# Kernel optimization log

Measured on AMD Instinct MI355X. Metric: run time of the kernel, lower is better.

Reference implementation:

```python
import jax, jax.numpy as jnp
import numpy as np
import math

B, T, D = 2, 2048, 1024
H, HD = 16, 64          # num_heads, head_dim = D // H
ROPE, BASE = 64, 10000.0  # rope covers full head dim
GLOBAL_IDS = jnp.array([2, 3, 4, 5, 6, 7], dtype=jnp.int32)


def setup_inputs() -> dict:
    key = jax.random.key(0)
    k1, k2, k3, k4 = jax.random.split(key, 4)
    x = jax.random.normal(k1, (B, T, D), dtype=jnp.float32)
    input_ids = jax.random.randint(k2, (B, T), 0, 1024, dtype=jnp.int32)
    W_qkv = jax.random.normal(k3, (3 * H * HD, D), dtype=jnp.float32) * 0.02
    b_qkv = jnp.zeros((3 * H * HD,), dtype=jnp.float32)
    W_out = jax.random.normal(k4, (D, H * HD), dtype=jnp.float32) * 0.02
    b_out = jnp.zeros((D,), dtype=jnp.float32)
    return {"x": x, "input_ids": input_ids, "W_qkv": W_qkv, "b_qkv": b_qkv,
            "W_out": W_out, "b_out": b_out}


def _apply_rotary(x, cos, sin):
    # x: [B,H,T,HD]; rope covers first ROPE dims (= full head here)
    x_rot, x_pass = x[..., :ROPE], x[..., ROPE:]
    half = ROPE // 2
    x1, x2 = x_rot[..., :half], x_rot[..., half:]
    x1n = x1 * cos - x2 * sin
    x2n = x1 * sin + x2 * cos
    return jnp.concatenate([x1n, x2n, x_pass], axis=-1)


def reference(x, input_ids, W_qkv, b_qkv, W_out, b_out):
    Bx, Tx, _ = x.shape
    qkv = x @ W_qkv.T + b_qkv                      # [B,T,3*H*HD]
    q, k, v = jnp.split(qkv, 3, axis=-1)
    def heads(t):
        return t.reshape(Bx, Tx, H, HD).transpose(0, 2, 1, 3)  # [B,H,T,HD]
    q, k, v = heads(q), heads(k), heads(v)

    # RoPE
    pos = jnp.arange(Tx, dtype=jnp.float32)
    inv_freq = 1.0 / (BASE ** (jnp.arange(0, ROPE, 2, dtype=jnp.float32) / ROPE))
    freqs = pos[:, None] * inv_freq[None, :]        # [T, ROPE//2]
    cos, sin = jnp.cos(freqs)[None, None], jnp.sin(freqs)[None, None]
    q = _apply_rotary(q, cos, sin)
    k = _apply_rotary(k, cos, sin)

    # causal mask OR global-query rows (BigBird-style)
    causal = jnp.tril(jnp.ones((Tx, Tx), dtype=bool))[None, None]   # [1,1,T,T]
    global_mask = jnp.isin(input_ids, GLOBAL_IDS)                    # [B,T]
    allow = causal | global_mask[:, None, :, None]                   # [B,1,T,T]

    scale = math.sqrt(HD)
    logits = jnp.einsum('bhqd,bhkd->bhqk', q, k) / scale
    neg = -jnp.finfo(logits.dtype).max
    logits = jnp.where(allow, logits, neg)
    attn = jax.nn.softmax(logits, axis=-1)
    out = jnp.einsum('bhqk,bhkd->bhqd', attn, v)
    out = out.transpose(0, 2, 1, 3).reshape(Bx, Tx, H * HD)
    return out @ W_out.T + b_out
```

## Files before the change

### kernel.cpp

```cpp
#include <hip/hip_runtime.h>
#include <math.h>

#define Bc 2
#define Tc 2048
#define Dc 1024
#define Hc 16
#define HDc 64

typedef __attribute__((ext_vector_type(8))) short bf16x8;
typedef __attribute__((ext_vector_type(4))) float f32x4;
typedef __attribute__((ext_vector_type(16))) float f32x16;

__device__ __forceinline__ unsigned short f2bf(float f) {
    union { float f; unsigned int u; } v; v.f = f;
    unsigned int r = (v.u + 0x7FFFu + ((v.u >> 16) & 1u)) >> 16;
    return (unsigned short)r;
}
__device__ __forceinline__ unsigned pack2bf(float a, float b) {
    unsigned au = __float_as_uint(a) + 0x8000u;
    unsigned bu = __float_as_uint(b) + 0x8000u;
    return __builtin_amdgcn_perm(bu, au, 0x07060302u);
}

#define CEXP 0.1803368801111204f

__global__ __launch_bounds__(256) void convert_bf16(
    const float* __restrict__ x, const float* __restrict__ wqkv,
    const float* __restrict__ wout,
    unsigned short* __restrict__ xb, unsigned short* __restrict__ wqkvb,
    unsigned short* __restrict__ woutb, float2* __restrict__ ropeTab)
{
    const int gid = blockIdx.x * 256 + threadIdx.x;
    if (gid < Tc * 32) {
        const int t = gid >> 5, i = gid & 31;
        const float freq = exp2f((float)i * -0.4152410118609203f);
        const float ang = (float)t * freq;
        ropeTab[gid] = make_float2(cosf(ang), sinf(ang));
    }
    const int i = gid * 4;
    const float* src; unsigned short* dst; int off;
    if (i < 4194304)      { src = x;    dst = xb;    off = i; }
    else if (i < 7340032) { src = wqkv; dst = wqkvb; off = i - 4194304; }
    else                  { src = wout; dst = woutb; off = i - 7340032; }
    float4 v = *(const float4*)&src[off];
    ushort4 o;
    o.x = f2bf(v.x); o.y = f2bf(v.y); o.z = f2bf(v.z); o.w = f2bf(v.w);
    *(ushort4*)&dst[off] = o;
}

template <int MODE>
__global__ __launch_bounds__(256) void gemm_mfma(
    const unsigned short* __restrict__ A, const unsigned short* __restrict__ W,
    const float* __restrict__ bias, float* __restrict__ C,
    unsigned short* __restrict__ Qp, unsigned short* __restrict__ Kp,
    unsigned short* __restrict__ Vtp, const float2* __restrict__ ropeTab,
    int M, int N, int K)
{
    __shared__ unsigned short Apk[128 * 8 * 8];
    __shared__ unsigned short Bpk[128 * 8 * 8];

    const int tid = threadIdx.x;
    const int lane = tid & 63;
    const int wave = tid >> 6;
    const int quad = lane >> 4;
    const int c = lane & 15;
    const int wm = wave >> 1;
    const int wn = wave & 1;
    const int m0 = blockIdx.y * 128;
    const int n0 = blockIdx.x * 128;

    f32x4 acc[4][4];
#pragma unroll
    for (int mt = 0; mt < 4; mt++)
#pragma unroll
        for (int nt = 0; nt < 4; nt++) acc[mt][nt] = (f32x4){0.f, 0.f, 0.f, 0.f};

    const int soct = tid & 7;
    const int srow0 = tid >> 3;

    for (int k0 = 0; k0 < K; k0 += 64) {
        __syncthreads();
#pragma unroll
        for (int it = 0; it < 4; it++) {
            const int row = srow0 + it * 32;
            bf16x8 av = *(const bf16x8*)&A[(size_t)(m0 + row) * K + k0 + soct * 8];
            *(bf16x8*)&Apk[(row * 8 + (soct ^ (row & 7))) * 8] = av;
            bf16x8 wv = *(const bf16x8*)&W[(size_t)(n0 + row) * K + k0 + soct * 8];
            *(bf16x8*)&Bpk[(row * 8 + (soct ^ (row & 7))) * 8] = wv;
        }
        __syncthreads();
#pragma unroll
        for (int ko = 0; ko < 2; ko++) {
            bf16x8 af[4], bf[4];
#pragma unroll
            for (int mt = 0; mt < 4; mt++) {
                const int m = wm * 64 + mt * 16 + c;
                af[mt] = *(const bf16x8*)&Apk[(m * 8 + ((ko * 4 + quad) ^ (m & 7))) * 8];
            }
#pragma unroll
            for (int nt = 0; nt < 4; nt++) {
                const int n = wn * 64 + nt * 16 + c;
                bf[nt] = *(const bf16x8*)&Bpk[(n * 8 + ((ko * 4 + quad) ^ (n & 7))) * 8];
            }
#pragma unroll
            for (int mt = 0; mt < 4; mt++)
#pragma unroll
                for (int nt = 0; nt < 4; nt++)
                    acc[mt][nt] = __builtin_amdgcn_mfma_f32_16x16x32_bf16(
                        af[mt], bf[nt], acc[mt][nt], 0, 0, 0);
        }
    }

    if (MODE == 0) {
#pragma unroll
        for (int mt = 0; mt < 4; mt++) {
            const int m = m0 + wm * 64 + mt * 16 + quad * 4;
#pragma unroll
            for (int nt = 0; nt < 4; nt++) {
                const int n = n0 + wn * 64 + nt * 16 + c;
                const float bv = bias[n];
#pragma unroll
                for (int reg = 0; reg < 4; reg++)
                    C[(size_t)(m + reg) * N + n] = acc[mt][nt][reg] + bv;
            }
        }
    } else {
        const int n_wave = n0 + wn * 64;
        const int which = n_wave >> 10;
        const int h = (n_wave >> 6) & 15;
        const int b = m0 >> 11;
        const int t_base = (m0 & 2047) + wm * 64;

        __syncthreads();
        unsigned short* stg = ((wave < 2) ? Apk : Bpk) + (wave & 1) * 4096;

        if (which < 2) {
            unsigned short* dst = (which == 0) ? Qp : Kp;
#pragma unroll
            for (int mt = 0; mt < 4; mt++) {
#pragma unroll
                for (int nt = 0; nt < 2; nt++) {
                    const int i1 = nt * 16 + c;
                    const float bv1 = bias[n_wave + i1];
                    const float bv2 = bias[n_wave + 32 + i1];
#pragma unroll
                    for (int reg = 0; reg < 4; reg++) {
                        const int row = mt * 16 + quad * 4 + reg;
                        const float2 cs = ropeTab[(t_base + row) * 32 + i1];
                        const float x1 = acc[mt][nt][reg] + bv1;
                        const float x2 = acc[mt][nt + 2][reg] + bv2;
                        const int col2 = 32 + i1;
                        stg[(row * 8 + ((i1 >> 3) ^ (row & 7))) * 8 + (i1 & 7)] =
                            f2bf(x1 * cs.x - x2 * cs.y);
                        stg[(row * 8 + ((col2 >> 3) ^ (row & 7))) * 8 + (col2 & 7)] =
                            f2bf(x1 * cs.y + x2 * cs.x);
                    }
                }
            }
            const size_t obase = ((size_t)(b * Hc + h) * Tc + t_base) * HDc;
            const int oct = lane & 7;
#pragma unroll
            for (int k = 0; k < 8; k++) {
                const int f = lane * 8 + k * 512;
                const int row = f >> 6;
                bf16x8 vv = *(const bf16x8*)&stg[(row * 8 + (oct ^ (row & 7))) * 8];
                *(bf16x8*)&dst[obase + f] = vv;
            }
        } else {
#pragma unroll
            for (int mt = 0; mt < 4; mt++) {
#pragma unroll
                for (int nt = 0; nt < 4; nt++) {
                    const int d = nt * 16 + c;
                    const float bv = bias[n_wave + d];
#pragma unroll
                    for (int reg = 0; reg < 4; reg++) {
                        const int r = mt * 16 + quad * 4 + reg;
                        stg[(d * 8 + ((r >> 3) ^ (d & 7))) * 8 + (r & 7)] =
                            f2bf(acc[mt][nt][reg] + bv);
                    }
                }
            }
            const size_t vbase = (size_t)(b * Hc + h) * HDc * Tc;
            const int oct = lane & 7;
#pragma unroll
            for (int k = 0; k < 8; k++) {
                const int d = (lane >> 3) + k * 8;
                bf16x8 vv = *(const bf16x8*)&stg[(d * 8 + (oct ^ (d & 7))) * 8];
                *(bf16x8*)&Vtp[vbase + (size_t)d * Tc + t_base + oct * 8] = vv;
            }
        }
    }
}

__global__ __launch_bounds__(256) void attn_fused(
    const unsigned short* __restrict__ Q, const unsigned short* __restrict__ K,
    const unsigned short* __restrict__ Vt, const int* __restrict__ ids,
    unsigned short* __restrict__ AO)
{
    __shared__ float smem[8448];

    const int tid = threadIdx.x;
    const int lane = tid & 63;
    const int wave = tid >> 6;
    const int c32 = lane & 31;
    const int h = lane >> 5;
    const int blk = blockIdx.x;

    if (blk < 32) {
        int* s_list = (int*)smem;
        int* s_cnt = (int*)smem + 64;
        float* s_accm = smem + 128;
        float* s_lm = s_accm + 8192;

        const int bh = blk;
        const int b = bh >> 4;
        const int hd = bh & 15;
        const size_t qkbase = (size_t)bh * Tc * HDc;

        if (tid == 0) *s_cnt = 0;
        __syncthreads();
        for (int i = tid; i < Tc; i += 256) {
            int id = ids[b * Tc + i];
            if ((unsigned)(id - 2) <= 5u) {
                int p = atomicAdd(s_cnt, 1);
                if (p < 64) s_list[p] = i;
            }
        }
        __syncthreads();
        const int cnt = min(*s_cnt, 64);

        for (int pass = 0; pass * 32 < cnt; pass++) {
            const int slot = pass * 32 + c32;
            const int row = (slot < cnt) ? s_list[slot] : s_list[0];

            bf16x8 qf[4];
#pragma unroll
            for (int ko = 0; ko < 4; ko++)
                qf[ko] = *(const bf16x8*)&Q[qkbase + (size_t)row * HDc + ko * 16 + h * 8];

            f32x16 acc0 = {}, acc1 = {};
            float lacc = 0.0f;

            for (int it = wave; it < Tc / 64; it += 4) {
                const int t0 = it * 64;
                f32x16 s0 = {}, s1 = {};
#pragma unroll
                for (int ko = 0; ko < 4; ko++) {
                    const int koff = ko * 16 + h * 8;
                    bf16x8 kf0 = *(const bf16x8*)&K[qkbase + (size_t)(t0 + c32) * HDc + koff];
                    bf16x8 kf1 = *(const bf16x8*)&K[qkbase + (size_t)(t0 + 32 + c32) * HDc + koff];
                    s0 = __builtin_amdgcn_mfma_f32_32x32x16_bf16(kf0, qf[ko], s0, 0, 0, 0);
                    s1 = __builtin_amdgcn_mfma_f32_32x32x16_bf16(kf1, qf[ko], s1, 0, 0, 0);
                }
                float v[32];
#pragma unroll
                for (int r = 0; r < 16; r++) { v[r] = s0[r]; v[16 + r] = s1[r]; }
#pragma unroll
                for (int i = 0; i < 32; i++) v[i] = exp2f(v[i] * CEXP);
                unsigned pk[16];
#pragma unroll
                for (int i = 0; i < 16; i++) pk[i] = pack2bf(v[2 * i], v[2 * i + 1]);
#pragma unroll
                for (int st = 1; st < 32; st <<= 1)
#pragma unroll
                    for (int i = 0; i < 32; i += 2 * st) v[i] += v[i + st];
                lacc += v[0];
#pragma unroll
                for (int ko = 0; ko < 4; ko++) {
                    const int a = (ko >> 1) * 8 + (ko & 1) * 4;
                    unsigned keep0 = h ? pk[a + 2] : pk[a + 0];
                    unsigned keep1 = h ? pk[a + 3] : pk[a + 1];
                    unsigned send0 = h ? pk[a + 0] : pk[a + 2];
                    unsigned send1 = h ? pk[a + 1] : pk[a + 3];
                    unsigned recv0 = (unsigned)__shfl_xor((int)send0, 32);
                    unsigned recv1 = (unsigned)__shfl_xor((int)send1, 32);
                    union { bf16x8 v8; unsigned u[4]; } pf;
                    pf.u[0] = h ? recv0 : keep0;
                    pf.u[1] = h ? recv1 : keep1;
                    pf.u[2] = h ? keep0 : recv0;
                    pf.u[3] = h ? keep1 : recv1;
                    const int oct = ko * 2 + h;
                    bf16x8 vf0 = *(const bf16x8*)&Vt[qkbase + (size_t)c32 * Tc + t0 + oct * 8];
                    bf16x8 vf1 = *(const bf16x8*)&Vt[qkbase + (size_t)(32 + c32) * Tc + t0 + oct * 8];
                    acc0 = __builtin_amdgcn_mfma_f32_32x32x16_bf16(vf0, pf.v8, acc0, 0, 0, 0);
                    acc1 = __builtin_amdgcn_mfma_f32_32x32x16_bf16(vf1, pf.v8, acc1, 0, 0, 0);
                }
            }

            const float lfull = lacc + __shfl_xor(lacc, 32);
            if (h == 0) s_lm[wave * 32 + c32] = lfull;
#pragma unroll
            for (int r = 0; r < 16; r++) {
                const int d = (r & 3) + 8 * (r >> 2) + 4 * h;
                s_accm[(wave * 64 + d) * 32 + c32] = acc0[r];
                s_accm[(wave * 64 + 32 + d) * 32 + c32] = acc1[r];
            }
            __syncthreads();
            for (int i = tid; i < 2048; i += 256) {
                const int sl = i >> 6, d = i & 63;
                if (pass * 32 + sl < cnt) {
                    const float o = s_accm[(0 * 64 + d) * 32 + sl] + s_accm[(1 * 64 + d) * 32 + sl] +
                                    s_accm[(2 * 64 + d) * 32 + sl] + s_accm[(3 * 64 + d) * 32 + sl];
                    const float lt = s_lm[sl] + s_lm[32 + sl] + s_lm[64 + sl] + s_lm[96 + sl];
                    const int qrow = s_list[pass * 32 + sl];
                    AO[((size_t)(b * Tc + qrow)) * Dc + hd * HDc + d] = f2bf(o / lt);
                }
            }
            __syncthreads();
        }
        return;
    }

    unsigned short* KV = (unsigned short*)smem;

    const int idx = blk - 32;
    const int bh = idx & 31;
    const int b = bh >> 4;
    const int hd = bh & 15;
    const int qi = 31 - (idx >> 5);
    const int qb0 = qi * 64;
    const int qsub = wave & 1;
    const int par = wave >> 1;
    const int wq0 = qb0 + qsub * 32;
    const size_t qkbase = (size_t)bh * Tc * HDc;
    const int q = wq0 + c32;

    bf16x8 qf[4];
#pragma unroll
    for (int ko = 0; ko < 4; ko++)
        qf[ko] = *(const bf16x8*)&Q[qkbase + (size_t)q * HDc + ko * 16 + h * 8];

    const int myid = ids[b * Tc + q];
    const bool gr = ((unsigned)(myid - 2) <= 5u);

    f32x16 acc0 = {}, acc1 = {};
    float lacc = 0.0f;

    const int nIter = qi + 1;
    const int skey = tid >> 3;
    const int soct = tid & 7;

    bf16x8 kA0, kA1, vA0, vA1, kB0, kB1, vB0, vB1;

    auto loadT = [&](int t0, bf16x8& k0, bf16x8& k1, bf16x8& v0, bf16x8& v1) {
        const int r0 = skey, r1 = skey + 32;
        k0 = *(const bf16x8*)&K[qkbase + (size_t)(t0 + r0) * HDc + soct * 8];
        k1 = *(const bf16x8*)&K[qkbase + (size_t)(t0 + r1) * HDc + soct * 8];
        v0 = *(const bf16x8*)&Vt[qkbase + (size_t)r0 * Tc + t0 + soct * 8];
        v1 = *(const bf16x8*)&Vt[qkbase + (size_t)r1 * Tc + t0 + soct * 8];
    };
    auto writeT = [&](int buf, bf16x8 k0, bf16x8 k1, bf16x8 v0, bf16x8 v1) {
        const int r0 = skey, r1 = skey + 32;
        unsigned short* Kb = KV + buf * 4096;
        unsigned short* Vb = KV + 8192 + buf * 4096;
        *(bf16x8*)&Kb[(r0 * 8 + (soct ^ (r0 & 7))) * 8] = k0;
        *(bf16x8*)&Kb[(r1 * 8 + (soct ^ (r1 & 7))) * 8] = k1;
        *(bf16x8*)&Vb[(r0 * 8 + (soct ^ (r0 & 7))) * 8] = v0;
        *(bf16x8*)&Vb[(r1 * 8 + (soct ^ (r1 & 7))) * 8] = v1;
    };

    auto compute = [&](int buf, int t0) {
        if (((t0 >> 6) & 1) != par) return;
        const unsigned short* Kb = KV + buf * 4096;
        const unsigned short* Vb = KV + 8192 + buf * 4096;

        f32x16 s0 = {}, s1 = {};
#pragma unroll
        for (int ko = 0; ko < 4; ko++) {
            const int oct = ko * 2 + h;
            const int k0i = c32;
            const int k1i = 32 + c32;
            bf16x8 kf0 = *(const bf16x8*)&Kb[(k0i * 8 + (oct ^ (k0i & 7))) * 8];
            bf16x8 kf1 = *(const bf16x8*)&Kb[(k1i * 8 + (oct ^ (k1i & 7))) * 8];
            s0 = __builtin_amdgcn_mfma_f32_32x32x16_bf16(kf0, qf[ko], s0, 0, 0, 0);
            s1 = __builtin_amdgcn_mfma_f32_32x32x16_bf16(kf1, qf[ko], s1, 0, 0, 0);
        }

        float v[32];
#pragma unroll
        for (int r = 0; r < 16; r++) { v[r] = s0[r]; v[16 + r] = s1[r]; }
#pragma unroll
        for (int i = 0; i < 32; i++) v[i] = exp2f(v[i] * CEXP);

        const bool needMask = (t0 + 63 > wq0);
        if (needMask) {
            const int thr = wq0 + c32 - t0 - 4 * h;
#pragma unroll
            for (int kt = 0; kt < 2; kt++)
#pragma unroll
                for (int r = 0; r < 16; r++) {
                    const int ckr = kt * 32 + (r & 3) + 8 * (r >> 2);
                    v[kt * 16 + r] = (ckr <= thr) ? v[kt * 16 + r] : 0.0f;
                }
        }

        unsigned pk[16];
#pragma unroll
        for (int i = 0; i < 16; i++) pk[i] = pack2bf(v[2 * i], v[2 * i + 1]);

#pragma unroll
        for (int st = 1; st < 32; st <<= 1)
#pragma unroll
            for (int i = 0; i < 32; i += 2 * st) v[i] += v[i + st];
        lacc += v[0];

#pragma unroll
        for (int ko = 0; ko < 4; ko++) {
            const int a = (ko >> 1) * 8 + (ko & 1) * 4;
            unsigned keep0 = h ? pk[a + 2] : pk[a + 0];
            unsigned keep1 = h ? pk[a + 3] : pk[a + 1];
            unsigned send0 = h ? pk[a + 0] : pk[a + 2];
            unsigned send1 = h ? pk[a + 1] : pk[a + 3];
            unsigned recv0 = (unsigned)__shfl_xor((int)send0, 32);
            unsigned recv1 = (unsigned)__shfl_xor((int)send1, 32);
            union { bf16x8 v8; unsigned u[4]; } pf;
            pf.u[0] = h ? recv0 : keep0;
            pf.u[1] = h ? recv1 : keep1;
            pf.u[2] = h ? keep0 : recv0;
            pf.u[3] = h ? keep1 : recv1;
            const int oct = ko * 2 + h;
            const int d0 = c32, d1 = 32 + c32;
            bf16x8 vf0 = *(const bf16x8*)&Vb[(d0 * 8 + (oct ^ (d0 & 7))) * 8];
            bf16x8 vf1 = *(const bf16x8*)&Vb[(d1 * 8 + (oct ^ (d1 & 7))) * 8];
            acc0 = __builtin_amdgcn_mfma_f32_32x32x16_bf16(vf0, pf.v8, acc0, 0, 0, 0);
            acc1 = __builtin_amdgcn_mfma_f32_32x32x16_bf16(vf1, pf.v8, acc1, 0, 0, 0);
        }
    };

    loadT(0, kA0, kA1, vA0, vA1);
    writeT(0, kA0, kA1, vA0, vA1);
    for (int it = 0; ; it += 2) {
        __syncthreads();
        const bool p1 = (it + 1) < nIter;
        if (p1) loadT((it + 1) * 64, kB0, kB1, vB0, vB1);
        compute(0, it * 64);
        if (!p1) break;
        writeT(1, kB0, kB1, vB0, vB1);
        __syncthreads();
        const bool p2 = (it + 2) < nIter;
        if (p2) loadT((it + 2) * 64, kA0, kA1, vA0, vA1);
        compute(1, (it + 1) * 64);
        if (!p2) break;
        writeT(0, kA0, kA1, vA0, vA1);
    }

    const float lw_ = lacc + __shfl_xor(lacc, 32);
    __syncthreads();
    float* mrg = smem;
    float* lmr = smem + 4096;
    if (wave >= 2) {
        const int s = wave - 2;
#pragma unroll
        for (int r = 0; r < 16; r++) {
            const int d = (r & 3) + 8 * (r >> 2) + 4 * h;
            mrg[(s * 64 + d) * 32 + c32] = acc0[r];
            mrg[(s * 64 + 32 + d) * 32 + c32] = acc1[r];
        }
        if (h == 0) lmr[s * 32 + c32] = lw_;
    }
    __syncthreads();
    if (wave < 2 && !gr) {
        const float l = lw_ + lmr[wave * 32 + c32];
        const float inv = 1.0f / l;
        unsigned short* dst = &AO[((size_t)(b * Tc + q)) * Dc + hd * HDc];
#pragma unroll
        for (int i = 0; i < 8; i++) {
            const int r = 2 * i;
            const int d = (r & 3) + 8 * (r >> 2) + 4 * h;
            const float a0 = acc0[r]     + mrg[(wave * 64 + d) * 32 + c32];
            const float a1 = acc0[r + 1] + mrg[(wave * 64 + d + 1) * 32 + c32];
            const float b0 = acc1[r]     + mrg[(wave * 64 + 32 + d) * 32 + c32];
            const float b1 = acc1[r + 1] + mrg[(wave * 64 + 32 + d + 1) * 32 + c32];
            *(unsigned*)&dst[d]      = pack2bf(a0 * inv, a1 * inv);
            *(unsigned*)&dst[32 + d] = pack2bf(b0 * inv, b1 * inv);
        }
    }
}

extern "C" void kernel_launch(void* const* d_in, const int* in_sizes, int n_in,
                              void* d_out, int out_size, void* d_ws, size_t ws_size,
                              hipStream_t stream)
{
    const float* x    = (const float*)d_in[0];
    const int*   ids  = (const int*)d_in[1];
    const float* Wqkv = (const float*)d_in[2];
    const float* bqkv = (const float*)d_in[3];
    const float* Wout = (const float*)d_in[4];
    const float* bout = (const float*)d_in[5];
    float* out = (float*)d_out;

    const size_t TEN = (size_t)Bc * Hc * Tc * HDc;
    unsigned short* xb    = (unsigned short*)d_ws;
    unsigned short* wqkvb = xb + 4194304;
    unsigned short* woutb = wqkvb + 3145728;
    float2* ropeTab       = (float2*)(woutb + 1048576);
    unsigned short* Qb    = (unsigned short*)(ropeTab + 65536);
    unsigned short* Kb    = Qb + TEN;
    unsigned short* Vtb   = Kb + TEN;
    unsigned short* AOb   = Vtb + TEN;

    convert_bf16<<<8192, 256, 0, stream>>>(x, Wqkv, Wout, xb, wqkvb, woutb,
                                           ropeTab);
    dim3 g1(3072 / 128, 4096 / 128);
    gemm_mfma<1><<<g1, 256, 0, stream>>>(xb, wqkvb, bqkv, nullptr,
                                         Qb, Kb, Vtb, ropeTab, 4096, 3072, 1024);
    attn_fused<<<1056, 256, 0, stream>>>(Qb, Kb, Vtb, ids, AOb);
    dim3 g4(1024 / 128, 4096 / 128);
    gemm_mfma<0><<<g4, 256, 0, stream>>>(AOb, woutb, bout, out,
                                         nullptr, nullptr, nullptr, nullptr,
                                         4096, 1024, 1024);
}
```

Before: 220.4 us.

## Give each wave its own 32-query block and stream K/V directly from global

The causal attention path drops the shared-memory K/V staging, the block-level double buffer and the cross-wave partial-sum merge. Each wave now owns one 32-row query group and walks every key tile itself, loading K fragments from global one tile ahead and V fragments straight into registers. The grid shrinks from 1056 to 544 blocks. This removes the __syncthreads barriers and the LDS merge, but each wave now reads the full K/V stream on its own, which multiplies global/L2 traffic and exposes more load latency. Register pressure also rises.

```diff
diff --git a/kernel.cpp b/kernel.cpp
--- a/kernel.cpp
+++ b/kernel.cpp
@@ -312,17 +312,12 @@
         return;
     }
 
-    unsigned short* KV = (unsigned short*)smem;
-
-    const int idx = blk - 32;
-    const int bh = idx & 31;
+    const int widx = (blk - 32) * 4 + wave;
+    const int bh = widx & 31;
     const int b = bh >> 4;
     const int hd = bh & 15;
-    const int qi = 31 - (idx >> 5);
-    const int qb0 = qi * 64;
-    const int qsub = wave & 1;
-    const int par = wave >> 1;
-    const int wq0 = qb0 + qsub * 32;
+    const int qg = 63 - (widx >> 5);
+    const int wq0 = qg * 32;
     const size_t qkbase = (size_t)bh * Tc * HDc;
     const int q = wq0 + c32;
 
@@ -336,45 +331,38 @@
 
     f32x16 acc0 = {}, acc1 = {};
     float lacc = 0.0f;
-
-    const int nIter = qi + 1;
-    const int skey = tid >> 3;
-    const int soct = tid & 7;
-
-    bf16x8 kA0, kA1, vA0, vA1, kB0, kB1, vB0, vB1;
-
-    auto loadT = [&](int t0, bf16x8& k0, bf16x8& k1, bf16x8& v0, bf16x8& v1) {
-        const int r0 = skey, r1 = skey + 32;
-        k0 = *(const bf16x8*)&K[qkbase + (size_t)(t0 + r0) * HDc + soct * 8];
-        k1 = *(const bf16x8*)&K[qkbase + (size_t)(t0 + r1) * HDc + soct * 8];
-        v0 = *(const bf16x8*)&Vt[qkbase + (size_t)r0 * Tc + t0 + soct * 8];
-        v1 = *(const bf16x8*)&Vt[qkbase + (size_t)r1 * Tc + t0 + soct * 8];
-    };
-    auto writeT = [&](int buf, bf16x8 k0, bf16x8 k1, bf16x8 v0, bf16x8 v1) {
-        const int r0 = skey, r1 = skey + 32;
-        unsigned short* Kb = KV + buf * 4096;
-        unsigned short* Vb = KV + 8192 + buf * 4096;
-        *(bf16x8*)&Kb[(r0 * 8 + (soct ^ (r0 & 7))) * 8] = k0;
-        *(bf16x8*)&Kb[(r1 * 8 + (soct ^ (r1 & 7))) * 8] = k1;
-        *(bf16x8*)&Vb[(r0 * 8 + (soct ^ (r0 & 7))) * 8] = v0;
-        *(bf16x8*)&Vb[(r1 * 8 + (soct ^ (r1 & 7))) * 8] = v1;
-    };
-
-    auto compute = [&](int buf, int t0) {
-        if (((t0 >> 6) & 1) != par) return;
-        const unsigned short* Kb = KV + buf * 4096;
-        const unsigned short* Vb = KV + 8192 + buf * 4096;
-
-        f32x16 s0 = {}, s1 = {};
+    const int nIter = (qg >> 1) + 1;
+
+    bf16x8 kcur[8], knext[8], vcur[8];
+#pragma unroll
+    for (int ko = 0; ko < 4; ko++) {
+        const int koff = ko * 16 + h * 8;
+        kcur[ko * 2 + 0] = *(const bf16x8*)&K[qkbase + (size_t)c32 * HDc + koff];
+        kcur[ko * 2 + 1] = *(const bf16x8*)&K[qkbase + (size_t)(32 + c32) * HDc + koff];
+    }
+
+    for (int it = 0; it < nIter; it++) {
+        const int t0 = it * 64;
 #pragma unroll
         for (int ko = 0; ko < 4; ko++) {
             const int oct = ko * 2 + h;
-            const int k0i = c32;
-            const int k1i = 32 + c32;
-            bf16x8 kf0 = *(const bf16x8*)&Kb[(k0i * 8 + (oct ^ (k0i & 7))) * 8];
-            bf16x8 kf1 = *(const bf16x8*)&Kb[(k1i * 8 + (oct ^ (k1i & 7))) * 8];
-            s0 = __builtin_amdgcn_mfma_f32_32x32x16_bf16(kf0, qf[ko], s0, 0, 0, 0);
-            s1 = __builtin_amdgcn_mfma_f32_32x32x16_bf16(kf1, qf[ko], s1, 0, 0, 0);
+            vcur[ko * 2 + 0] = *(const bf16x8*)&Vt[qkbase + (size_t)c32 * Tc + t0 + oct * 8];
+            vcur[ko * 2 + 1] = *(const bf16x8*)&Vt[qkbase + (size_t)(32 + c32) * Tc + t0 + oct * 8];
+        }
+        if (it + 1 < nIter) {
+#pragma unroll
+            for (int ko = 0; ko < 4; ko++) {
+                const int koff = ko * 16 + h * 8;
+                knext[ko * 2 + 0] = *(const bf16x8*)&K[qkbase + (size_t)(t0 + 64 + c32) * HDc + koff];
+                knext[ko * 2 + 1] = *(const bf16x8*)&K[qkbase + (size_t)(t0 + 96 + c32) * HDc + koff];
+            }
+        }
+
+        f32x16 s0 = {}, s1 = {};
+#pragma unroll
+        for (int ko = 0; ko < 4; ko++) {
+            s0 = __builtin_amdgcn_mfma_f32_32x32x16_bf16(kcur[ko * 2 + 0], qf[ko], s0, 0, 0, 0);
+            s1 = __builtin_amdgcn_mfma_f32_32x32x16_bf16(kcur[ko * 2 + 1], qf[ko], s1, 0, 0, 0);
         }
 
         float v[32];
@@ -419,61 +407,23 @@
             pf.u[1] = h ? recv1 : keep1;
             pf.u[2] = h ? keep0 : recv0;
             pf.u[3] = h ? keep1 : recv1;
-            const int oct = ko * 2 + h;
-            const int d0 = c32, d1 = 32 + c32;
-            bf16x8 vf0 = *(const bf16x8*)&Vb[(d0 * 8 + (oct ^ (d0 & 7))) * 8];
-            bf16x8 vf1 = *(const bf16x8*)&Vb[(d1 * 8 + (oct ^ (d1 & 7))) * 8];
-            acc0 = __builtin_amdgcn_mfma_f32_32x32x16_bf16(vf0, pf.v8, acc0, 0, 0, 0);
-            acc1 = __builtin_amdgcn_mfma_f32_32x32x16_bf16(vf1, pf.v8, acc1, 0, 0, 0);
-        }
-    };
-
-    loadT(0, kA0, kA1, vA0, vA1);
-    writeT(0, kA0, kA1, vA0, vA1);
-    for (int it = 0; ; it += 2) {
-        __syncthreads();
-        const bool p1 = (it + 1) < nIter;
-        if (p1) loadT((it + 1) * 64, kB0, kB1, vB0, vB1);
-        compute(0, it * 64);
-        if (!p1) break;
-        writeT(1, kB0, kB1, vB0, vB1);
-        __syncthreads();
-        const bool p2 = (it + 2) < nIter;
-        if (p2) loadT((it + 2) * 64, kA0, kA1, vA0, vA1);
-        compute(1, (it + 1) * 64);
-        if (!p2) break;
-        writeT(0, kA0, kA1, vA0, vA1);
-    }
-
-    const float lw_ = lacc + __shfl_xor(lacc, 32);
-    __syncthreads();
-    float* mrg = smem;
-    float* lmr = smem + 4096;
-    if (wave >= 2) {
-        const int s = wave - 2;
-#pragma unroll
-        for (int r = 0; r < 16; r++) {
-            const int d = (r & 3) + 8 * (r >> 2) + 4 * h;
-            mrg[(s * 64 + d) * 32 + c32] = acc0[r];
-            mrg[(s * 64 + 32 + d) * 32 + c32] = acc1[r];
-        }
-        if (h == 0) lmr[s * 32 + c32] = lw_;
-    }
-    __syncthreads();
-    if (wave < 2 && !gr) {
-        const float l = lw_ + lmr[wave * 32 + c32];
+            acc0 = __builtin_amdgcn_mfma_f32_32x32x16_bf16(vcur[ko * 2 + 0], pf.v8, acc0, 0, 0, 0);
+            acc1 = __builtin_amdgcn_mfma_f32_32x32x16_bf16(vcur[ko * 2 + 1], pf.v8, acc1, 0, 0, 0);
+        }
+#pragma unroll
+        for (int i = 0; i < 8; i++) kcur[i] = knext[i];
+    }
+
+    const float l = lacc + __shfl_xor(lacc, 32);
+    if (!gr) {
         const float inv = 1.0f / l;
         unsigned short* dst = &AO[((size_t)(b * Tc + q)) * Dc + hd * HDc];
 #pragma unroll
         for (int i = 0; i < 8; i++) {
             const int r = 2 * i;
             const int d = (r & 3) + 8 * (r >> 2) + 4 * h;
-            const float a0 = acc0[r]     + mrg[(wave * 64 + d) * 32 + c32];
-            const float a1 = acc0[r + 1] + mrg[(wave * 64 + d + 1) * 32 + c32];
-            const float b0 = acc1[r]     + mrg[(wave * 64 + 32 + d) * 32 + c32];
-            const float b1 = acc1[r + 1] + mrg[(wave * 64 + 32 + d + 1) * 32 + c32];
-            *(unsigned*)&dst[d]      = pack2bf(a0 * inv, a1 * inv);
-            *(unsigned*)&dst[32 + d] = pack2bf(b0 * inv, b1 * inv);
+            *(unsigned*)&dst[d]      = pack2bf(acc0[r] * inv, acc0[r + 1] * inv);
+            *(unsigned*)&dst[32 + d] = pack2bf(acc1[r] * inv, acc1[r + 1] * inv);
         }
     }
 }
@@ -505,7 +455,7 @@
     dim3 g1(3072 / 128, 4096 / 128);
     gemm_mfma<1><<<g1, 256, 0, stream>>>(xb, wqkvb, bqkv, nullptr,
                                          Qb, Kb, Vtb, ropeTab, 4096, 3072, 1024);
-    attn_fused<<<1056, 256, 0, stream>>>(Qb, Kb, Vtb, ids, AOb);
+    attn_fused<<<544, 256, 0, stream>>>(Qb, Kb, Vtb, ids, AOb);
     dim3 g4(1024 / 128, 4096 / 128);
     gemm_mfma<0><<<g4, 256, 0, stream>>>(AOb, woutb, bout, out,
                                          nullptr, nullptr, nullptr, nullptr,
```

Result: slower. 245.1 us (+11.2%).

## Give each attention wave its own 32 queries over a 128-row block

Applied to the files above, without the earlier changes.

The causal attention blocks now cover 128 query rows, with each of the four waves owning 32 distinct queries. Previously two pairs of waves split the key tiles by parity and merged partial accumulators through shared memory. This removes the cross-wave merge, its extra barriers and shared-memory traffic, and halves the number of attention blocks so each K/V tile load serves more queries. The trade-offs are fewer blocks (544 vs 1056), less parallelism, and waves that idle on key tiles past their causal limit.

```diff
diff --git a/kernel.cpp b/kernel.cpp
--- a/kernel.cpp
+++ b/kernel.cpp
@@ -318,11 +318,9 @@
     const int bh = idx & 31;
     const int b = bh >> 4;
     const int hd = bh & 15;
-    const int qi = 31 - (idx >> 5);
-    const int qb0 = qi * 64;
-    const int qsub = wave & 1;
-    const int par = wave >> 1;
-    const int wq0 = qb0 + qsub * 32;
+    const int qb = 15 - (idx >> 5);
+    const int qb0 = qb * 128;
+    const int wq0 = qb0 + wave * 32;
     const size_t qkbase = (size_t)bh * Tc * HDc;
     const int q = wq0 + c32;
 
@@ -337,7 +335,7 @@
     f32x16 acc0 = {}, acc1 = {};
     float lacc = 0.0f;
 
-    const int nIter = qi + 1;
+    const int nIter = 2 * qb + 2;
     const int skey = tid >> 3;
     const int soct = tid & 7;
 
@@ -361,7 +359,7 @@
     };
 
     auto compute = [&](int buf, int t0) {
-        if (((t0 >> 6) & 1) != par) return;
+        if (t0 > wq0 + 31) return;
         const unsigned short* Kb = KV + buf * 4096;
         const unsigned short* Vb = KV + 8192 + buf * 4096;
 
@@ -445,35 +443,16 @@
         writeT(0, kA0, kA1, vA0, vA1);
     }
 
-    const float lw_ = lacc + __shfl_xor(lacc, 32);
-    __syncthreads();
-    float* mrg = smem;
-    float* lmr = smem + 4096;
-    if (wave >= 2) {
-        const int s = wave - 2;
-#pragma unroll
-        for (int r = 0; r < 16; r++) {
-            const int d = (r & 3) + 8 * (r >> 2) + 4 * h;
-            mrg[(s * 64 + d) * 32 + c32] = acc0[r];
-            mrg[(s * 64 + 32 + d) * 32 + c32] = acc1[r];
-        }
-        if (h == 0) lmr[s * 32 + c32] = lw_;
-    }
-    __syncthreads();
-    if (wave < 2 && !gr) {
-        const float l = lw_ + lmr[wave * 32 + c32];
+    const float l = lacc + __shfl_xor(lacc, 32);
+    if (!gr) {
         const float inv = 1.0f / l;
         unsigned short* dst = &AO[((size_t)(b * Tc + q)) * Dc + hd * HDc];
 #pragma unroll
         for (int i = 0; i < 8; i++) {
             const int r = 2 * i;
             const int d = (r & 3) + 8 * (r >> 2) + 4 * h;
-            const float a0 = acc0[r]     + mrg[(wave * 64 + d) * 32 + c32];
-            const float a1 = acc0[r + 1] + mrg[(wave * 64 + d + 1) * 32 + c32];
-            const float b0 = acc1[r]     + mrg[(wave * 64 + 32 + d) * 32 + c32];
-            const float b1 = acc1[r + 1] + mrg[(wave * 64 + 32 + d + 1) * 32 + c32];
-            *(unsigned*)&dst[d]      = pack2bf(a0 * inv, a1 * inv);
-            *(unsigned*)&dst[32 + d] = pack2bf(b0 * inv, b1 * inv);
+            *(unsigned*)&dst[d]      = pack2bf(acc0[r] * inv, acc0[r + 1] * inv);
+            *(unsigned*)&dst[32 + d] = pack2bf(acc1[r] * inv, acc1[r + 1] * inv);
         }
     }
 }
@@ -505,7 +484,7 @@
     dim3 g1(3072 / 128, 4096 / 128);
     gemm_mfma<1><<<g1, 256, 0, stream>>>(xb, wqkvb, bqkv, nullptr,
                                          Qb, Kb, Vtb, ropeTab, 4096, 3072, 1024);
-    attn_fused<<<1056, 256, 0, stream>>>(Qb, Kb, Vtb, ids, AOb);
+    attn_fused<<<544, 256, 0, stream>>>(Qb, Kb, Vtb, ids, AOb);
     dim3 g4(1024 / 128, 4096 / 128);
     gemm_mfma<0><<<g4, 256, 0, stream>>>(AOb, woutb, bout, out,
                                          nullptr, nullptr, nullptr, nullptr,
```

After: 202.2 us. -8.2%, faster.
